# Optimization experiments

Hardware: AMD Instinct MI355X
Metric: run time of the kernel (lower is better)

## Reference

```python
import jax, jax.numpy as jnp
import numpy as np

T = 32
BATCH = 1024
LATENT = 1024
HIDDEN = 1024


def setup_inputs() -> dict:
    key = jax.random.key(0)
    ks = jax.random.split(key, 13)
    s = 0.02
    return {
        "latent": jax.random.normal(ks[0], (BATCH, LATENT), jnp.float32),
        "h0": jax.random.normal(ks[1], (BATCH, HIDDEN), jnp.float32),
        "c0": jax.random.normal(ks[2], (BATCH, HIDDEN), jnp.float32),
        # LSTM kernel (input dim = 2*LATENT), recurrent kernel, bias; gate order i,f,g,o
        "Wk": jax.random.normal(ks[3], (2 * LATENT, 4 * HIDDEN), jnp.float32) * s,
        "Wr": jax.random.normal(ks[4], (HIDDEN, 4 * HIDDEN), jnp.float32) * s,
        "b": jnp.zeros((4 * HIDDEN,), jnp.float32),
        # attention: w1 on latent, w2 on concat(h,c)
        "W1": jax.random.normal(ks[5], (LATENT, LATENT), jnp.float32) * s,
        "b1": jnp.zeros((LATENT,), jnp.float32),
        "W2": jax.random.normal(ks[6], (2 * HIDDEN, LATENT), jnp.float32) * s,
        "b2": jnp.zeros((LATENT,), jnp.float32),
        # output mu dense
        "Wmu": jax.random.normal(ks[7], (HIDDEN, 1), jnp.float32) * s,
        "bmu": jnp.zeros((1,), jnp.float32),
    }


def _attention_context(h, c, latent, W1, b1, W2, b2):
    # score: (batch, latent_dims); softmax over feature axis (axis=1) as in the original
    query = jnp.concatenate([h, c], axis=-1)
    score = jnp.tanh(latent @ W1 + b1 + query @ W2 + b2)
    beta = jax.nn.softmax(score, axis=1)
    return beta * latent


def reference(latent, h0, c0, Wk, Wr, b, W1, b1, W2, b2, Wmu, bmu):
    # initial attention/context from h0, c0
    context = _attention_context(h0, c0, latent, W1, b1, W2, b2)

    def step(carry, _):
        h, c, ctx = carry
        x = jnp.concatenate([latent, ctx], axis=-1)  # (batch, 2*latent)
        z = x @ Wk + h @ Wr + b                       # (batch, 4*hidden)
        i, f, g, o = jnp.split(z, 4, axis=-1)         # keras gate order i,f,c,o
        c_new = jax.nn.sigmoid(f) * c + jax.nn.sigmoid(i) * jnp.tanh(g)
        h_new = jax.nn.sigmoid(o) * jnp.tanh(c_new)
        ctx_new = _attention_context(h_new, c_new, latent, W1, b1, W2, b2)
        out = h_new @ Wmu + bmu                        # (batch, 1)
        return (h_new, c_new, ctx_new), out

    _, outs = jax.lax.scan(step, (h0, c0, context), None, length=T)
    # outs: (T, batch, 1) -> (batch, T, 1)
    return jnp.transpose(outs, (1, 0, 2))
```

## Files before the change

kernel.cpp:

```cpp
#include <hip/hip_runtime.h>


#define T_ 32

typedef __attribute__((ext_vector_type(8))) short short8;
typedef __attribute__((ext_vector_type(4))) float f32x4;

__device__ __forceinline__ unsigned short bf16u(float x) {
  unsigned int u = __float_as_uint(x);
  u += 0x7FFFu + ((u >> 16) & 1u);
  return (unsigned short)(u >> 16);
}
__device__ __forceinline__ float b2f(unsigned short u) {
  return __uint_as_float(((unsigned int)u) << 16);
}
__device__ __forceinline__ ushort4 pack4(float a, float b, float c, float d) {
  ushort4 v; v.x = bf16u(a); v.y = bf16u(b); v.z = bf16u(c); v.w = bf16u(d); return v;
}
__device__ __forceinline__ float sigmoidf_(float x) { return 1.f / (1.f + __expf(-x)); }
__device__ __forceinline__ float tanhf_(float x) { return 1.f - 2.f / (__expf(2.f * x) + 1.f); }

__global__ void k_transpose(const float* __restrict__ src, int srcN,
                            unsigned short* __restrict__ dst, int dstStride, int dstColOff) {
  __shared__ float tile[32][33];
  int n0 = blockIdx.x * 32, k0 = blockIdx.y * 32;
  int tx = threadIdx.x, ty = threadIdx.y;
#pragma unroll
  for (int i = 0; i < 4; ++i)
    tile[ty + i * 8][tx] = src[(size_t)(k0 + ty + i * 8) * srcN + n0 + tx];
  __syncthreads();
#pragma unroll
  for (int i = 0; i < 4; ++i)
    dst[(size_t)(n0 + ty + i * 8) * dstStride + dstColOff + k0 + tx] = bf16u(tile[tx][ty + i * 8]);
}

__global__ __launch_bounds__(256) void k_init(const float* __restrict__ h0,
                                              const float* __restrict__ c0,
                                              const float* __restrict__ latent,
                                              unsigned short* __restrict__ A1,
                                              unsigned short* __restrict__ A2,
                                              unsigned short* __restrict__ latbf,
                                              float* __restrict__ c_st) {
  int r = blockIdx.x; int j = threadIdx.x * 4;
  const float4 hv = *(const float4*)&h0[(size_t)r * 1024 + j];
  const float4 cv = *(const float4*)&c0[(size_t)r * 1024 + j];
  const float4 lv = *(const float4*)&latent[(size_t)r * 1024 + j];
  *(ushort4*)&A2[(size_t)r * 2048 + j]        = pack4(hv.x, hv.y, hv.z, hv.w);
  *(ushort4*)&A2[(size_t)r * 2048 + 1024 + j] = pack4(cv.x, cv.y, cv.z, cv.w);
  *(ushort4*)&A1[(size_t)r * 2048 + 1024 + j] = pack4(hv.x, hv.y, hv.z, hv.w);
  *(ushort4*)&latbf[(size_t)r * 1024 + j]     = pack4(lv.x, lv.y, lv.z, lv.w);
  *(float4*)&c_st[(size_t)r * 1024 + j] = cv;
}

__global__ void k_bias(const float* __restrict__ b1, const float* __restrict__ b2,
                       float* __restrict__ bias_s) {
  int i = blockIdx.x * 256 + threadIdx.x;
  bias_s[i] = b1[i] + b2[i];
}

__global__ __launch_bounds__(256) void k_gemm(const unsigned short* __restrict__ A, int lda,
                                              const unsigned short* __restrict__ Bt, int ldb,
                                              int Kchunk,
                                              const float* __restrict__ bias,
                                              unsigned short* __restrict__ Cb, int N) {
  __shared__ unsigned short Al[2][128 * 64];
  __shared__ unsigned short Bl[2][128 * 64];
  const int tid = threadIdx.x;
  const int w = tid >> 6, l = tid & 63;
  const int row0 = blockIdx.y * 128, col0 = blockIdx.x * 128;
  const int wr = (w >> 1) * 64, wc = (w & 1) * 64;
  const int lr = l & 15;
  const int srow = (l >> 3);
  const int scol_src = ((l & 7) ^ srow) * 8;
  const int kbeg = blockIdx.z * Kchunk;
  const int nsteps = Kchunk >> 6;

  f32x4 acc[4][4] = {};

  auto stage = [&](int buf, int k0) {
#pragma unroll
    for (int it = 0; it < 4; ++it) {
      int chunk = w * 4 + it;
      int r = chunk * 8 + srow;
      const unsigned short* ga = A + (size_t)(row0 + r) * lda + k0 + scol_src;
      const unsigned short* gb = Bt + (size_t)(col0 + r) * ldb + k0 + scol_src;
      __builtin_amdgcn_global_load_lds(
          (const __attribute__((address_space(1))) unsigned int*)ga,
          (__attribute__((address_space(3))) unsigned int*)((char*)&Al[buf][0] + chunk * 1024), 16, 0, 0);
      __builtin_amdgcn_global_load_lds(
          (const __attribute__((address_space(1))) unsigned int*)gb,
          (__attribute__((address_space(3))) unsigned int*)((char*)&Bl[buf][0] + chunk * 1024), 16, 0, 0);
    }
  };

  stage(0, kbeg);
  __syncthreads();
  int cur = 0;
  for (int s = 0; s < nsteps; ++s) {
    if (s + 1 < nsteps) stage(cur ^ 1, kbeg + (s + 1) * 64);
#pragma unroll
    for (int kk = 0; kk < 2; ++kk) {
      const int c2 = kk * 64 + (l >> 4) * 16;
      short8 a[4], b[4];
#pragma unroll
      for (int m = 0; m < 4; ++m) {
        int r = wr + m * 16 + lr;
        a[m] = *(const short8*)((char*)&Al[cur][0] + r * 128 + (c2 ^ ((r & 7) << 4)));
      }
#pragma unroll
      for (int n = 0; n < 4; ++n) {
        int r = wc + n * 16 + lr;
        b[n] = *(const short8*)((char*)&Bl[cur][0] + r * 128 + (c2 ^ ((r & 7) << 4)));
      }
#pragma unroll
      for (int m = 0; m < 4; ++m)
#pragma unroll
        for (int n = 0; n < 4; ++n)
          acc[m][n] = __builtin_amdgcn_mfma_f32_16x16x32_bf16(a[m], b[n], acc[m][n], 0, 0, 0);
    }
    __syncthreads();
    cur ^= 1;
  }

  const int rbase = (l >> 4) * 4;
  unsigned short* Cp = Cb + (size_t)blockIdx.z * (size_t)(gridDim.y * 128) * N;
#pragma unroll
  for (int m = 0; m < 4; ++m)
#pragma unroll
    for (int rg = 0; rg < 4; ++rg) {
      int row = row0 + wr + m * 16 + rbase + rg;
#pragma unroll
      for (int n = 0; n < 4; ++n) {
        int col = col0 + wc + n * 16 + lr;
        float v = acc[m][n][rg];
        if (bias) v += bias[col];
        Cp[(size_t)row * N + col] = bf16u(v);
      }
    }
}

__global__ __launch_bounds__(256) void k_lstm(const unsigned short* __restrict__ z_latb,
                                              const unsigned short* __restrict__ zp,
                                              float* __restrict__ c_st,
                                              unsigned short* __restrict__ A1,
                                              unsigned short* __restrict__ A2,
                                              const float* __restrict__ Wmu,
                                              const float* __restrict__ bmu,
                                              float* __restrict__ out, int t) {
  __shared__ float red[4];
  const size_t Z1 = (size_t)1024 * 4096;
  int r = blockIdx.x; int tid = threadIdx.x; int j = tid * 4;
  float g4[4][4];
#pragma unroll
  for (int g = 0; g < 4; ++g) {
    const ushort4 zl = *(const ushort4*)&z_latb[(size_t)r * 4096 + g * 1024 + j];
    const ushort4 p0 = *(const ushort4*)&zp[(size_t)r * 4096 + g * 1024 + j];
    const ushort4 p1 = *(const ushort4*)&zp[Z1 + (size_t)r * 4096 + g * 1024 + j];
    g4[g][0] = b2f(zl.x) + b2f(p0.x) + b2f(p1.x);
    g4[g][1] = b2f(zl.y) + b2f(p0.y) + b2f(p1.y);
    g4[g][2] = b2f(zl.z) + b2f(p0.z) + b2f(p1.z);
    g4[g][3] = b2f(zl.w) + b2f(p0.w) + b2f(p1.w);
  }
  const float4 cv = *(const float4*)&c_st[(size_t)r * 1024 + j];
  const float4 wm = *(const float4*)&Wmu[j];
  float cc[4] = {cv.x, cv.y, cv.z, cv.w}, wv[4] = {wm.x, wm.y, wm.z, wm.w};
  float cn[4], hn[4];
  float part = 0.f;
#pragma unroll
  for (int q = 0; q < 4; ++q) {
    float c2 = sigmoidf_(g4[1][q]) * cc[q] + sigmoidf_(g4[0][q]) * tanhf_(g4[2][q]);
    float h2 = sigmoidf_(g4[3][q]) * tanhf_(c2);
    cn[q] = c2; hn[q] = h2; part += h2 * wv[q];
  }
  *(float4*)&c_st[(size_t)r * 1024 + j] = make_float4(cn[0], cn[1], cn[2], cn[3]);
  *(ushort4*)&A2[(size_t)r * 2048 + j]        = pack4(hn[0], hn[1], hn[2], hn[3]);
  *(ushort4*)&A2[(size_t)r * 2048 + 1024 + j] = pack4(cn[0], cn[1], cn[2], cn[3]);
  *(ushort4*)&A1[(size_t)r * 2048 + 1024 + j] = pack4(hn[0], hn[1], hn[2], hn[3]);
#pragma unroll
  for (int off = 32; off > 0; off >>= 1) part += __shfl_down(part, off, 64);
  if ((tid & 63) == 0) red[tid >> 6] = part;
  __syncthreads();
  if (tid == 0) out[(size_t)r * T_ + t] = red[0] + red[1] + red[2] + red[3] + bmu[0];
}

__global__ __launch_bounds__(256) void k_attn(const unsigned short* __restrict__ s_latb,
                                              const unsigned short* __restrict__ sp8,
                                              const float* __restrict__ latent,
                                              unsigned short* __restrict__ A1) {
  __shared__ float red[4];
  const size_t P = (size_t)1024 * 1024;
  int r = blockIdx.x; int tid = threadIdx.x; int j = tid * 4;
  const ushort4 sl = *(const ushort4*)&s_latb[(size_t)r * 1024 + j];
  float sv[4] = {b2f(sl.x), b2f(sl.y), b2f(sl.z), b2f(sl.w)};
#pragma unroll
  for (int sidx = 0; sidx < 8; ++sidx) {
    const ushort4 q = *(const ushort4*)&sp8[sidx * P + (size_t)r * 1024 + j];
    sv[0] += b2f(q.x); sv[1] += b2f(q.y); sv[2] += b2f(q.z); sv[3] += b2f(q.w);
  }
  float s[4] = {tanhf_(sv[0]), tanhf_(sv[1]), tanhf_(sv[2]), tanhf_(sv[3])};
  float mx = fmaxf(fmaxf(s[0], s[1]), fmaxf(s[2], s[3]));
#pragma unroll
  for (int off = 32; off > 0; off >>= 1) mx = fmaxf(mx, __shfl_xor(mx, off, 64));
  if ((tid & 63) == 0) red[tid >> 6] = mx;
  __syncthreads();
  mx = fmaxf(fmaxf(red[0], red[1]), fmaxf(red[2], red[3]));
  __syncthreads();
  float e[4], ps = 0.f;
#pragma unroll
  for (int q = 0; q < 4; ++q) { e[q] = __expf(s[q] - mx); ps += e[q]; }
#pragma unroll
  for (int off = 32; off > 0; off >>= 1) ps += __shfl_xor(ps, off, 64);
  if ((tid & 63) == 0) red[tid >> 6] = ps;
  __syncthreads();
  float inv = 1.f / (red[0] + red[1] + red[2] + red[3]);
  const float4 lv = *(const float4*)&latent[(size_t)r * 1024 + j];
  *(ushort4*)&A1[(size_t)r * 2048 + j] =
      pack4(e[0] * inv * lv.x, e[1] * inv * lv.y, e[2] * inv * lv.z, e[3] * inv * lv.w);
}

extern "C" void kernel_launch(void* const* d_in, const int* in_sizes, int n_in,
                              void* d_out, int out_size, void* d_ws, size_t ws_size,
                              hipStream_t stream) {
  const float* latent = (const float*)d_in[0];
  const float* h0  = (const float*)d_in[1];
  const float* c0  = (const float*)d_in[2];
  const float* Wk  = (const float*)d_in[3];
  const float* Wr  = (const float*)d_in[4];
  const float* b   = (const float*)d_in[5];
  const float* W1  = (const float*)d_in[6];
  const float* b1  = (const float*)d_in[7];
  const float* W2  = (const float*)d_in[8];
  const float* b2  = (const float*)d_in[9];
  const float* Wmu = (const float*)d_in[10];
  const float* bmu = (const float*)d_in[11];
  float* out = (float*)d_out;

  char* p = (char*)d_ws;
  auto alloc = [&](size_t bytes) { void* r = (void*)p; p += (bytes + 255) & ~(size_t)255; return r; };
  unsigned short* Wzh_t = (unsigned short*)alloc((size_t)4096 * 2048 * 2);
  unsigned short* Wk1_t = (unsigned short*)alloc((size_t)4096 * 1024 * 2);
  unsigned short* W1t   = (unsigned short*)alloc((size_t)1024 * 1024 * 2);
  unsigned short* W2t   = (unsigned short*)alloc((size_t)1024 * 2048 * 2);
  unsigned short* latbf = (unsigned short*)alloc((size_t)1024 * 1024 * 2);
  unsigned short* A1    = (unsigned short*)alloc((size_t)1024 * 2048 * 2);
  unsigned short* A2    = (unsigned short*)alloc((size_t)1024 * 2048 * 2);
  unsigned short* z_latb = (unsigned short*)alloc((size_t)1024 * 4096 * 2);
  unsigned short* s_latb = (unsigned short*)alloc((size_t)1024 * 1024 * 2);
  unsigned short* z_part = (unsigned short*)alloc((size_t)2 * 1024 * 4096 * 2);
  unsigned short* spre_p = (unsigned short*)alloc((size_t)8 * 1024 * 1024 * 2);
  float* c_st   = (float*)alloc((size_t)1024 * 1024 * 4);
  float* bias_s = (float*)alloc((size_t)1024 * 4);

  dim3 tb(32, 8);
  k_transpose<<<dim3(128, 32), tb, 0, stream>>>(Wk, 4096, Wk1_t, 1024, 0);
  k_transpose<<<dim3(128, 32), tb, 0, stream>>>(Wk + (size_t)1024 * 4096, 4096, Wzh_t, 2048, 0);
  k_transpose<<<dim3(128, 32), tb, 0, stream>>>(Wr, 4096, Wzh_t, 2048, 1024);
  k_transpose<<<dim3(32, 64), tb, 0, stream>>>(W2, 1024, W2t, 2048, 0);
  k_transpose<<<dim3(32, 32), tb, 0, stream>>>(W1, 1024, W1t, 1024, 0);

  k_init<<<1024, 256, 0, stream>>>(h0, c0, latent, A1, A2, latbf, c_st);
  k_bias<<<4, 256, 0, stream>>>(b1, b2, bias_s);

  k_gemm<<<dim3(32, 8, 1), 256, 0, stream>>>(latbf, 1024, Wk1_t, 1024, 1024, b, z_latb, 4096);
  k_gemm<<<dim3(8, 8, 1), 256, 0, stream>>>(latbf, 1024, W1t, 1024, 1024, bias_s, s_latb, 1024);

  k_gemm<<<dim3(8, 8, 8), 256, 0, stream>>>(A2, 2048, W2t, 2048, 256, nullptr, spre_p, 1024);
  k_attn<<<1024, 256, 0, stream>>>(s_latb, spre_p, latent, A1);

  for (int t = 0; t < T_; ++t) {
    k_gemm<<<dim3(32, 8, 2), 256, 0, stream>>>(A1, 2048, Wzh_t, 2048, 1024, nullptr, z_part, 4096);
    k_lstm<<<1024, 256, 0, stream>>>(z_latb, z_part, c_st, A1, A2, Wmu, bmu, out, t);
    if (t < T_ - 1) {
      k_gemm<<<dim3(8, 8, 8), 256, 0, stream>>>(A2, 2048, W2t, 2048, 256, nullptr, spre_p, 1024);
      k_attn<<<1024, 256, 0, stream>>>(s_latb, spre_p, latent, A1);
    }
  }
}
```

Baseline: 1.650 ms.

## Single-buffer GEMM LDS and double split-K for recurrent and attention GEMMs

The GEMM kernel drops LDS double buffering and uses a single load-sync-compute-sync loop, which halves LDS use per block so more blocks can be resident. Split-K is doubled for the per-step LSTM GEMM (2 to 4) and the attention GEMM (8 to 16), which raises block counts to fill more CUs. The consumer kernels now sum 4 and 16 bf16 partials. In exchange, global loads no longer overlap with MFMA work within a block, more partial-sum traffic is written and read, and summing more bf16-rounded partials adds rounding error.

```diff
diff --git a/kernel.cpp b/kernel.cpp
--- a/kernel.cpp
+++ b/kernel.cpp
@@ -63,8 +63,8 @@
                                               int Kchunk,
                                               const float* __restrict__ bias,
                                               unsigned short* __restrict__ Cb, int N) {
-  __shared__ unsigned short Al[2][128 * 64];
-  __shared__ unsigned short Bl[2][128 * 64];
+  __shared__ unsigned short Al[128 * 64];
+  __shared__ unsigned short Bl[128 * 64];
   const int tid = threadIdx.x;
   const int w = tid >> 6, l = tid & 63;
   const int row0 = blockIdx.y * 128, col0 = blockIdx.x * 128;
@@ -77,7 +77,8 @@
 
   f32x4 acc[4][4] = {};
 
-  auto stage = [&](int buf, int k0) {
+  for (int s = 0; s < nsteps; ++s) {
+    const int k0 = kbeg + s * 64;
 #pragma unroll
     for (int it = 0; it < 4; ++it) {
       int chunk = w * 4 + it;
@@ -86,18 +87,12 @@
       const unsigned short* gb = Bt + (size_t)(col0 + r) * ldb + k0 + scol_src;
       __builtin_amdgcn_global_load_lds(
           (const __attribute__((address_space(1))) unsigned int*)ga,
-          (__attribute__((address_space(3))) unsigned int*)((char*)&Al[buf][0] + chunk * 1024), 16, 0, 0);
+          (__attribute__((address_space(3))) unsigned int*)((char*)Al + chunk * 1024), 16, 0, 0);
       __builtin_amdgcn_global_load_lds(
           (const __attribute__((address_space(1))) unsigned int*)gb,
-          (__attribute__((address_space(3))) unsigned int*)((char*)&Bl[buf][0] + chunk * 1024), 16, 0, 0);
-    }
-  };
-
-  stage(0, kbeg);
-  __syncthreads();
-  int cur = 0;
-  for (int s = 0; s < nsteps; ++s) {
-    if (s + 1 < nsteps) stage(cur ^ 1, kbeg + (s + 1) * 64);
+          (__attribute__((address_space(3))) unsigned int*)((char*)Bl + chunk * 1024), 16, 0, 0);
+    }
+    __syncthreads();
 #pragma unroll
     for (int kk = 0; kk < 2; ++kk) {
       const int c2 = kk * 64 + (l >> 4) * 16;
@@ -105,12 +100,12 @@
 #pragma unroll
       for (int m = 0; m < 4; ++m) {
         int r = wr + m * 16 + lr;
-        a[m] = *(const short8*)((char*)&Al[cur][0] + r * 128 + (c2 ^ ((r & 7) << 4)));
+        a[m] = *(const short8*)((char*)Al + r * 128 + (c2 ^ ((r & 7) << 4)));
       }
 #pragma unroll
       for (int n = 0; n < 4; ++n) {
         int r = wc + n * 16 + lr;
-        b[n] = *(const short8*)((char*)&Bl[cur][0] + r * 128 + (c2 ^ ((r & 7) << 4)));
+        b[n] = *(const short8*)((char*)Bl + r * 128 + (c2 ^ ((r & 7) << 4)));
       }
 #pragma unroll
       for (int m = 0; m < 4; ++m)
@@ -119,7 +114,6 @@
           acc[m][n] = __builtin_amdgcn_mfma_f32_16x16x32_bf16(a[m], b[n], acc[m][n], 0, 0, 0);
     }
     __syncthreads();
-    cur ^= 1;
   }
 
   const int rbase = (l >> 4) * 4;
@@ -148,18 +142,19 @@
                                               const float* __restrict__ bmu,
                                               float* __restrict__ out, int t) {
   __shared__ float red[4];
-  const size_t Z1 = (size_t)1024 * 4096;
+  const size_t Z = (size_t)1024 * 4096;
   int r = blockIdx.x; int tid = threadIdx.x; int j = tid * 4;
   float g4[4][4];
 #pragma unroll
   for (int g = 0; g < 4; ++g) {
     const ushort4 zl = *(const ushort4*)&z_latb[(size_t)r * 4096 + g * 1024 + j];
-    const ushort4 p0 = *(const ushort4*)&zp[(size_t)r * 4096 + g * 1024 + j];
-    const ushort4 p1 = *(const ushort4*)&zp[Z1 + (size_t)r * 4096 + g * 1024 + j];
-    g4[g][0] = b2f(zl.x) + b2f(p0.x) + b2f(p1.x);
-    g4[g][1] = b2f(zl.y) + b2f(p0.y) + b2f(p1.y);
-    g4[g][2] = b2f(zl.z) + b2f(p0.z) + b2f(p1.z);
-    g4[g][3] = b2f(zl.w) + b2f(p0.w) + b2f(p1.w);
+    float s0 = b2f(zl.x), s1 = b2f(zl.y), s2 = b2f(zl.z), s3 = b2f(zl.w);
+#pragma unroll
+    for (int zi = 0; zi < 4; ++zi) {
+      const ushort4 pv = *(const ushort4*)&zp[zi * Z + (size_t)r * 4096 + g * 1024 + j];
+      s0 += b2f(pv.x); s1 += b2f(pv.y); s2 += b2f(pv.z); s3 += b2f(pv.w);
+    }
+    g4[g][0] = s0; g4[g][1] = s1; g4[g][2] = s2; g4[g][3] = s3;
   }
   const float4 cv = *(const float4*)&c_st[(size_t)r * 1024 + j];
   const float4 wm = *(const float4*)&Wmu[j];
@@ -184,7 +179,7 @@
 }
 
 __global__ __launch_bounds__(256) void k_attn(const unsigned short* __restrict__ s_latb,
-                                              const unsigned short* __restrict__ sp8,
+                                              const unsigned short* __restrict__ sp,
                                               const float* __restrict__ latent,
                                               unsigned short* __restrict__ A1) {
   __shared__ float red[4];
@@ -193,8 +188,8 @@
   const ushort4 sl = *(const ushort4*)&s_latb[(size_t)r * 1024 + j];
   float sv[4] = {b2f(sl.x), b2f(sl.y), b2f(sl.z), b2f(sl.w)};
 #pragma unroll
-  for (int sidx = 0; sidx < 8; ++sidx) {
-    const ushort4 q = *(const ushort4*)&sp8[sidx * P + (size_t)r * 1024 + j];
+  for (int sidx = 0; sidx < 16; ++sidx) {
+    const ushort4 q = *(const ushort4*)&sp[sidx * P + (size_t)r * 1024 + j];
     sv[0] += b2f(q.x); sv[1] += b2f(q.y); sv[2] += b2f(q.z); sv[3] += b2f(q.w);
   }
   float s[4] = {tanhf_(sv[0]), tanhf_(sv[1]), tanhf_(sv[2]), tanhf_(sv[3])};
@@ -246,8 +241,8 @@
   unsigned short* A2    = (unsigned short*)alloc((size_t)1024 * 2048 * 2);
   unsigned short* z_latb = (unsigned short*)alloc((size_t)1024 * 4096 * 2);
   unsigned short* s_latb = (unsigned short*)alloc((size_t)1024 * 1024 * 2);
-  unsigned short* z_part = (unsigned short*)alloc((size_t)2 * 1024 * 4096 * 2);
-  unsigned short* spre_p = (unsigned short*)alloc((size_t)8 * 1024 * 1024 * 2);
+  unsigned short* z_part = (unsigned short*)alloc((size_t)4 * 1024 * 4096 * 2);
+  unsigned short* spre_p = (unsigned short*)alloc((size_t)16 * 1024 * 1024 * 2);
   float* c_st   = (float*)alloc((size_t)1024 * 1024 * 4);
   float* bias_s = (float*)alloc((size_t)1024 * 4);
 
@@ -264,14 +259,14 @@
   k_gemm<<<dim3(32, 8, 1), 256, 0, stream>>>(latbf, 1024, Wk1_t, 1024, 1024, b, z_latb, 4096);
   k_gemm<<<dim3(8, 8, 1), 256, 0, stream>>>(latbf, 1024, W1t, 1024, 1024, bias_s, s_latb, 1024);
 
-  k_gemm<<<dim3(8, 8, 8), 256, 0, stream>>>(A2, 2048, W2t, 2048, 256, nullptr, spre_p, 1024);
+  k_gemm<<<dim3(8, 8, 16), 256, 0, stream>>>(A2, 2048, W2t, 2048, 128, nullptr, spre_p, 1024);
   k_attn<<<1024, 256, 0, stream>>>(s_latb, spre_p, latent, A1);
 
   for (int t = 0; t < T_; ++t) {
-    k_gemm<<<dim3(32, 8, 2), 256, 0, stream>>>(A1, 2048, Wzh_t, 2048, 1024, nullptr, z_part, 4096);
+    k_gemm<<<dim3(32, 8, 4), 256, 0, stream>>>(A1, 2048, Wzh_t, 2048, 512, nullptr, z_part, 4096);
     k_lstm<<<1024, 256, 0, stream>>>(z_latb, z_part, c_st, A1, A2, Wmu, bmu, out, t);
     if (t < T_ - 1) {
-      k_gemm<<<dim3(8, 8, 8), 256, 0, stream>>>(A2, 2048, W2t, 2048, 256, nullptr, spre_p, 1024);
+      k_gemm<<<dim3(8, 8, 16), 256, 0, stream>>>(A2, 2048, W2t, 2048, 128, nullptr, spre_p, 1024);
       k_attn<<<1024, 256, 0, stream>>>(s_latb, spre_p, latent, A1);
     }
   }
```

Result: slower. 2.110 ms (+27.9%).

## Deepen GEMM LDS pipeline to four stages with explicit vmcnt waits

Applied to the files above, without the earlier changes.

Reworks the bf16 MFMA GEMM main loop from a double-buffered 64-wide K tile to a four-buffer ring of 32-wide K tiles, keeping three loads in flight. Each step waits with an explicit s_waitcnt vmcnt plus a raw s_barrier instead of __syncthreads. The LDS swizzle and staging layout change to match the 16-row, 64-byte chunks. The aim is to hide global-to-LDS latency better across the many small recurrent GEMMs. The cost is more barriers per unit of K and fewer MFMAs per barrier, and correctness now rests on the hand-counted vmcnt values.

```diff
diff --git a/kernel.cpp b/kernel.cpp
--- a/kernel.cpp
+++ b/kernel.cpp
@@ -58,68 +58,72 @@
   bias_s[i] = b1[i] + b2[i];
 }
 
+#define GLD(src, dst)                                                                   \
+  __builtin_amdgcn_global_load_lds(                                                     \
+      (const __attribute__((address_space(1))) unsigned int*)(src),                     \
+      (__attribute__((address_space(3))) unsigned int*)(dst), 16, 0, 0)
+
 __global__ __launch_bounds__(256) void k_gemm(const unsigned short* __restrict__ A, int lda,
                                               const unsigned short* __restrict__ Bt, int ldb,
                                               int Kchunk,
                                               const float* __restrict__ bias,
                                               unsigned short* __restrict__ Cb, int N) {
-  __shared__ unsigned short Al[2][128 * 64];
-  __shared__ unsigned short Bl[2][128 * 64];
+  __shared__ unsigned short Al[4][128 * 32];
+  __shared__ unsigned short Bl[4][128 * 32];
   const int tid = threadIdx.x;
   const int w = tid >> 6, l = tid & 63;
   const int row0 = blockIdx.y * 128, col0 = blockIdx.x * 128;
   const int wr = (w >> 1) * 64, wc = (w & 1) * 64;
   const int lr = l & 15;
-  const int srow = (l >> 3);
-  const int scol_src = ((l & 7) ^ srow) * 8;
+  const int srow16 = l >> 2;
+  const int scol_src = ((l & 3) ^ (srow16 & 3)) * 8;
   const int kbeg = blockIdx.z * Kchunk;
-  const int nsteps = Kchunk >> 6;
+  const int nsteps = Kchunk >> 5;
 
   f32x4 acc[4][4] = {};
 
   auto stage = [&](int buf, int k0) {
 #pragma unroll
-    for (int it = 0; it < 4; ++it) {
-      int chunk = w * 4 + it;
-      int r = chunk * 8 + srow;
-      const unsigned short* ga = A + (size_t)(row0 + r) * lda + k0 + scol_src;
-      const unsigned short* gb = Bt + (size_t)(col0 + r) * ldb + k0 + scol_src;
-      __builtin_amdgcn_global_load_lds(
-          (const __attribute__((address_space(1))) unsigned int*)ga,
-          (__attribute__((address_space(3))) unsigned int*)((char*)&Al[buf][0] + chunk * 1024), 16, 0, 0);
-      __builtin_amdgcn_global_load_lds(
-          (const __attribute__((address_space(1))) unsigned int*)gb,
-          (__attribute__((address_space(3))) unsigned int*)((char*)&Bl[buf][0] + chunk * 1024), 16, 0, 0);
+    for (int it = 0; it < 2; ++it) {
+      int chunk = w * 2 + it;
+      int r = chunk * 16 + srow16;
+      GLD(A + (size_t)(row0 + r) * lda + k0 + scol_src, (char*)&Al[buf][0] + chunk * 1024);
+      GLD(Bt + (size_t)(col0 + r) * ldb + k0 + scol_src, (char*)&Bl[buf][0] + chunk * 1024);
     }
   };
 
   stage(0, kbeg);
-  __syncthreads();
-  int cur = 0;
+  if (nsteps > 1) stage(1, kbeg + 32);
+  if (nsteps > 2) stage(2, kbeg + 64);
+
   for (int s = 0; s < nsteps; ++s) {
-    if (s + 1 < nsteps) stage(cur ^ 1, kbeg + (s + 1) * 64);
-#pragma unroll
-    for (int kk = 0; kk < 2; ++kk) {
-      const int c2 = kk * 64 + (l >> 4) * 16;
-      short8 a[4], b[4];
-#pragma unroll
-      for (int m = 0; m < 4; ++m) {
-        int r = wr + m * 16 + lr;
-        a[m] = *(const short8*)((char*)&Al[cur][0] + r * 128 + (c2 ^ ((r & 7) << 4)));
-      }
-#pragma unroll
-      for (int n = 0; n < 4; ++n) {
-        int r = wc + n * 16 + lr;
-        b[n] = *(const short8*)((char*)&Bl[cur][0] + r * 128 + (c2 ^ ((r & 7) << 4)));
-      }
-#pragma unroll
-      for (int m = 0; m < 4; ++m)
-#pragma unroll
-        for (int n = 0; n < 4; ++n)
-          acc[m][n] = __builtin_amdgcn_mfma_f32_16x16x32_bf16(a[m], b[n], acc[m][n], 0, 0, 0);
-    }
-    __syncthreads();
-    cur ^= 1;
+    if (s + 2 < nsteps)      asm volatile("s_waitcnt vmcnt(8)" ::: "memory");
+    else if (s + 1 < nsteps) asm volatile("s_waitcnt vmcnt(4)" ::: "memory");
+    else                     asm volatile("s_waitcnt vmcnt(0)" ::: "memory");
+    __builtin_amdgcn_sched_barrier(0);
+    __builtin_amdgcn_s_barrier();
+
+    const int buf = s & 3;
+    const int c2 = (l >> 4) * 16;
+    short8 a[4], b[4];
+#pragma unroll
+    for (int m = 0; m < 4; ++m) {
+      int chunk_base = ((wr + m * 16) >> 4) * 1024;
+      a[m] = *(const short8*)((char*)&Al[buf][0] + chunk_base + lr * 64 + (c2 ^ ((lr & 3) << 4)));
+    }
+#pragma unroll
+    for (int n = 0; n < 4; ++n) {
+      int chunk_base = ((wc + n * 16) >> 4) * 1024;
+      b[n] = *(const short8*)((char*)&Bl[buf][0] + chunk_base + lr * 64 + (c2 ^ ((lr & 3) << 4)));
+    }
+#pragma unroll
+    for (int m = 0; m < 4; ++m)
+#pragma unroll
+      for (int n = 0; n < 4; ++n)
+        acc[m][n] = __builtin_amdgcn_mfma_f32_16x16x32_bf16(a[m], b[n], acc[m][n], 0, 0, 0);
+
+    __builtin_amdgcn_s_barrier();
+    if (s + 3 < nsteps) stage((s + 3) & 3, kbeg + (s + 3) * 32);
   }
 
   const int rbase = (l >> 4) * 4;
```

Result: slower. 1.836 ms (+11.3%).

## Triple-buffer GEMM LDS staging and reduce split-K partitions

Applied to the files above, without the earlier changes.

The GEMM kernel moves from double to triple buffering of LDS tiles. Loads are issued two steps ahead, and the code waits on vmcnt instead of a full __syncthreads, so global-to-LDS transfers overlap more of the MFMA work. The split-K factor is cut from 2 to 1 for the recurrent gate GEMM and from 8 to 4 for the attention GEMM, with the consumer kernels updated to sum fewer partials. This reduces partial-sum traffic and reduction work, at the cost of fewer blocks (256 each) and more LDS per block, which may lower occupancy and parallelism.

```diff
diff --git a/kernel.cpp b/kernel.cpp
--- a/kernel.cpp
+++ b/kernel.cpp
@@ -63,8 +63,8 @@
                                               int Kchunk,
                                               const float* __restrict__ bias,
                                               unsigned short* __restrict__ Cb, int N) {
-  __shared__ unsigned short Al[2][128 * 64];
-  __shared__ unsigned short Bl[2][128 * 64];
+  __shared__ unsigned short Al[3][128 * 64];
+  __shared__ unsigned short Bl[3][128 * 64];
   const int tid = threadIdx.x;
   const int w = tid >> 6, l = tid & 63;
   const int row0 = blockIdx.y * 128, col0 = blockIdx.x * 128;
@@ -94,10 +94,15 @@
   };
 
   stage(0, kbeg);
-  __syncthreads();
-  int cur = 0;
+  if (nsteps > 1) stage(1, kbeg + 64);
+
+  int buf = 0;
   for (int s = 0; s < nsteps; ++s) {
-    if (s + 1 < nsteps) stage(cur ^ 1, kbeg + (s + 1) * 64);
+    if (s + 1 < nsteps) asm volatile("s_waitcnt vmcnt(8)" ::: "memory");
+    else                asm volatile("s_waitcnt vmcnt(0)" ::: "memory");
+    __builtin_amdgcn_sched_barrier(0);
+    __builtin_amdgcn_s_barrier();
+    __builtin_amdgcn_sched_barrier(0);
 #pragma unroll
     for (int kk = 0; kk < 2; ++kk) {
       const int c2 = kk * 64 + (l >> 4) * 16;
@@ -105,12 +110,12 @@
 #pragma unroll
       for (int m = 0; m < 4; ++m) {
         int r = wr + m * 16 + lr;
-        a[m] = *(const short8*)((char*)&Al[cur][0] + r * 128 + (c2 ^ ((r & 7) << 4)));
+        a[m] = *(const short8*)((char*)&Al[buf][0] + r * 128 + (c2 ^ ((r & 7) << 4)));
       }
 #pragma unroll
       for (int n = 0; n < 4; ++n) {
         int r = wc + n * 16 + lr;
-        b[n] = *(const short8*)((char*)&Bl[cur][0] + r * 128 + (c2 ^ ((r & 7) << 4)));
+        b[n] = *(const short8*)((char*)&Bl[buf][0] + r * 128 + (c2 ^ ((r & 7) << 4)));
       }
 #pragma unroll
       for (int m = 0; m < 4; ++m)
@@ -118,8 +123,9 @@
         for (int n = 0; n < 4; ++n)
           acc[m][n] = __builtin_amdgcn_mfma_f32_16x16x32_bf16(a[m], b[n], acc[m][n], 0, 0, 0);
     }
-    __syncthreads();
-    cur ^= 1;
+    __builtin_amdgcn_s_barrier();
+    if (s + 2 < nsteps) stage((buf + 2 == 3) ? 0 : ((buf + 2 == 4) ? 1 : buf + 2), kbeg + (s + 2) * 64);
+    buf = (buf == 2) ? 0 : buf + 1;
   }
 
   const int rbase = (l >> 4) * 4;
@@ -148,18 +154,16 @@
                                               const float* __restrict__ bmu,
                                               float* __restrict__ out, int t) {
   __shared__ float red[4];
-  const size_t Z1 = (size_t)1024 * 4096;
   int r = blockIdx.x; int tid = threadIdx.x; int j = tid * 4;
   float g4[4][4];
 #pragma unroll
   for (int g = 0; g < 4; ++g) {
     const ushort4 zl = *(const ushort4*)&z_latb[(size_t)r * 4096 + g * 1024 + j];
     const ushort4 p0 = *(const ushort4*)&zp[(size_t)r * 4096 + g * 1024 + j];
-    const ushort4 p1 = *(const ushort4*)&zp[Z1 + (size_t)r * 4096 + g * 1024 + j];
-    g4[g][0] = b2f(zl.x) + b2f(p0.x) + b2f(p1.x);
-    g4[g][1] = b2f(zl.y) + b2f(p0.y) + b2f(p1.y);
-    g4[g][2] = b2f(zl.z) + b2f(p0.z) + b2f(p1.z);
-    g4[g][3] = b2f(zl.w) + b2f(p0.w) + b2f(p1.w);
+    g4[g][0] = b2f(zl.x) + b2f(p0.x);
+    g4[g][1] = b2f(zl.y) + b2f(p0.y);
+    g4[g][2] = b2f(zl.z) + b2f(p0.z);
+    g4[g][3] = b2f(zl.w) + b2f(p0.w);
   }
   const float4 cv = *(const float4*)&c_st[(size_t)r * 1024 + j];
   const float4 wm = *(const float4*)&Wmu[j];
@@ -184,7 +188,7 @@
 }
 
 __global__ __launch_bounds__(256) void k_attn(const unsigned short* __restrict__ s_latb,
-                                              const unsigned short* __restrict__ sp8,
+                                              const unsigned short* __restrict__ sp4,
                                               const float* __restrict__ latent,
                                               unsigned short* __restrict__ A1) {
   __shared__ float red[4];
@@ -193,8 +197,8 @@
   const ushort4 sl = *(const ushort4*)&s_latb[(size_t)r * 1024 + j];
   float sv[4] = {b2f(sl.x), b2f(sl.y), b2f(sl.z), b2f(sl.w)};
 #pragma unroll
-  for (int sidx = 0; sidx < 8; ++sidx) {
-    const ushort4 q = *(const ushort4*)&sp8[sidx * P + (size_t)r * 1024 + j];
+  for (int sidx = 0; sidx < 4; ++sidx) {
+    const ushort4 q = *(const ushort4*)&sp4[sidx * P + (size_t)r * 1024 + j];
     sv[0] += b2f(q.x); sv[1] += b2f(q.y); sv[2] += b2f(q.z); sv[3] += b2f(q.w);
   }
   float s[4] = {tanhf_(sv[0]), tanhf_(sv[1]), tanhf_(sv[2]), tanhf_(sv[3])};
@@ -246,8 +250,8 @@
   unsigned short* A2    = (unsigned short*)alloc((size_t)1024 * 2048 * 2);
   unsigned short* z_latb = (unsigned short*)alloc((size_t)1024 * 4096 * 2);
   unsigned short* s_latb = (unsigned short*)alloc((size_t)1024 * 1024 * 2);
-  unsigned short* z_part = (unsigned short*)alloc((size_t)2 * 1024 * 4096 * 2);
-  unsigned short* spre_p = (unsigned short*)alloc((size_t)8 * 1024 * 1024 * 2);
+  unsigned short* z_part = (unsigned short*)alloc((size_t)1024 * 4096 * 2);
+  unsigned short* spre_p = (unsigned short*)alloc((size_t)4 * 1024 * 1024 * 2);
   float* c_st   = (float*)alloc((size_t)1024 * 1024 * 4);
   float* bias_s = (float*)alloc((size_t)1024 * 4);
 
@@ -264,14 +268,14 @@
   k_gemm<<<dim3(32, 8, 1), 256, 0, stream>>>(latbf, 1024, Wk1_t, 1024, 1024, b, z_latb, 4096);
   k_gemm<<<dim3(8, 8, 1), 256, 0, stream>>>(latbf, 1024, W1t, 1024, 1024, bias_s, s_latb, 1024);
 
-  k_gemm<<<dim3(8, 8, 8), 256, 0, stream>>>(A2, 2048, W2t, 2048, 256, nullptr, spre_p, 1024);
+  k_gemm<<<dim3(8, 8, 4), 256, 0, stream>>>(A2, 2048, W2t, 2048, 512, nullptr, spre_p, 1024);
   k_attn<<<1024, 256, 0, stream>>>(s_latb, spre_p, latent, A1);
 
   for (int t = 0; t < T_; ++t) {
-    k_gemm<<<dim3(32, 8, 2), 256, 0, stream>>>(A1, 2048, Wzh_t, 2048, 1024, nullptr, z_part, 4096);
+    k_gemm<<<dim3(32, 8, 1), 256, 0, stream>>>(A1, 2048, Wzh_t, 2048, 2048, nullptr, z_part, 4096);
     k_lstm<<<1024, 256, 0, stream>>>(z_latb, z_part, c_st, A1, A2, Wmu, bmu, out, t);
     if (t < T_ - 1) {
-      k_gemm<<<dim3(8, 8, 8), 256, 0, stream>>>(A2, 2048, W2t, 2048, 256, nullptr, spre_p, 1024);
+      k_gemm<<<dim3(8, 8, 4), 256, 0, stream>>>(A2, 2048, W2t, 2048, 512, nullptr, spre_p, 1024);
       k_attn<<<1024, 256, 0, stream>>>(s_latb, spre_p, latent, A1);
     }
   }
```

New measurement: 1.987 ms. +20.4%, slower.
